# Optimization experiments

Hardware: AMD Instinct MI355X
Metric: run time of the kernel (lower is better)

Reference implementation:

```python
import jax, jax.numpy as jnp
import numpy as np

B, L, D, H, NL = 4, 2048, 128, 4, 2
DH = D // H
FF = 2 * D
EPS_LN = 1e-5


def _p(key, shape, scale=0.05):
    return (jax.random.normal(key, shape, dtype=jnp.float32) * scale)


def setup_inputs() -> dict:
    key = jax.random.key(0)
    ks = jax.random.split(key, 40)
    inp = {
        "local_global": jax.random.normal(ks[0], (B, D), dtype=jnp.float32),
        "task_features": jax.random.normal(ks[1], (B, L, 15), dtype=jnp.float32),
        "privacy_features": jax.random.normal(ks[2], (B, L, 6), dtype=jnp.float32),
        "dag_features": jax.random.normal(ks[3], (B, L, 4), dtype=jnp.float32),
        # float mask in [0,1); values > 0.5 are MASKED (set to -inf) per torch code
        "attn_mask": jax.random.uniform(ks[4], (B, L, L), dtype=jnp.float32),
        # input projections (stored [in, out]; torch Linear does x @ W.T + b)
        "task_W": _p(ks[5], (15, D)), "task_b": jnp.zeros((D,), jnp.float32),
        "priv_W": _p(ks[6], (6, D)), "priv_b": jnp.zeros((D,), jnp.float32),
        "dag_W": _p(ks[7], (4, D)), "dag_b": jnp.zeros((D,), jnp.float32),
        "pre_g": jnp.ones((D,), jnp.float32), "pre_b": jnp.zeros((D,), jnp.float32),
        "post_g": jnp.ones((D,), jnp.float32), "post_b": jnp.zeros((D,), jnp.float32),
        "out_W": _p(ks[8], (D, D)), "out_b": jnp.zeros((D,), jnp.float32),
        # per-layer params stacked on leading NL axis
        "qW": _p(ks[9], (NL, D, D)), "qb": jnp.zeros((NL, D), jnp.float32),
        "kW": _p(ks[10], (NL, D, D)), "kb": jnp.zeros((NL, D), jnp.float32),
        "vW": _p(ks[11], (NL, D, D)), "vb": jnp.zeros((NL, D), jnp.float32),
        "oW": _p(ks[12], (NL, D, D)), "ob": jnp.zeros((NL, D), jnp.float32),
        "n1g": jnp.ones((NL, D), jnp.float32), "n1b": jnp.zeros((NL, D), jnp.float32),
        "n2g": jnp.ones((NL, D), jnp.float32), "n2b": jnp.zeros((NL, D), jnp.float32),
        "f1W": _p(ks[13], (NL, D, FF)), "f1b": jnp.zeros((NL, FF), jnp.float32),
        "f2W": _p(ks[14], (NL, FF, D)), "f2b": jnp.zeros((NL, D), jnp.float32),
    }
    return inp


def _layernorm(x, g, b):
    mu = x.mean(-1, keepdims=True)
    var = ((x - mu) ** 2).mean(-1, keepdims=True)
    return (x - mu) * jax.lax.rsqrt(var + EPS_LN) * g + b


def _attention(x, add_mask, Wq, bq, Wk, bk, Wv, bv, Wo, bo):
    # x: [B,L,D]; add_mask: [B,L,L] additive (0 or -inf)
    def heads(y):
        return y.reshape(B, L, H, DH).transpose(0, 2, 1, 3)  # [B,H,L,DH]
    q = heads(x @ Wq + bq)
    k = heads(x @ Wk + bk)
    v = heads(x @ Wv + bv)
    scale = 1.0 / np.sqrt(DH).astype(np.float32)
    scores = jnp.einsum('bhqd,bhkd->bhqk', q, k) * scale + add_mask[:, None]
    # fully-masked-row diagonal fixup (torch: set diag score to 0 where row max is -inf)
    row_max = scores.max(-1)                       # [B,H,L]
    fully_masked = jnp.isinf(row_max) & (row_max < 0)
    eye = jnp.eye(L, dtype=bool)
    scores = jnp.where(fully_masked[..., None] & eye, 0.0, scores)
    w = jax.nn.softmax(scores, axis=-1)
    # NaN fallback: if any NaN, replace with 1/L and renormalize (applied globally, as torch does)
    has_nan = jnp.isnan(w).any()
    fixed = jnp.nan_to_num(w, nan=1.0 / L)
    fixed = fixed / (fixed.sum(-1, keepdims=True) + 1e-8)
    w = jnp.where(has_nan, fixed, w)
    out = jnp.einsum('bhqk,bhkd->bhqd', w, v)      # [B,H,L,DH]
    out = out.transpose(0, 2, 1, 3).reshape(B, L, D)
    return out @ Wo + bo


def reference(local_global, task_features, privacy_features, dag_features, attn_mask,
              task_W, task_b, priv_W, priv_b, dag_W, dag_b,
              pre_g, pre_b, post_g, post_b, out_W, out_b,
              qW, qb, kW, kb, vW, vb, oW, ob,
              n1g, n1b, n2g, n2b, f1W, f1b, f2W, f2b):
    # normalize mask: >0.5 means masked; fix all-False rows by masking their diagonal (torch quirk)
    mb = attn_mask > 0.5                            # [B,L,L] bool, True = mask out
    need_fix = ~mb.any(-1)                          # [B,L]
    eye = jnp.eye(L, dtype=bool)
    mb = mb | (need_fix[..., None] & eye)
    add_mask = jnp.where(mb, -jnp.inf, 0.0).astype(jnp.float32)

    ctx = (task_features @ task_W + task_b) + (privacy_features @ priv_W + priv_b) \
          + (dag_features @ dag_W + dag_b)
    x = _layernorm(ctx, pre_g, pre_b)
    for i in range(NL):  # eval mode: dropout = identity
        sa = _attention(_layernorm(x, n1g[i], n1b[i]), add_mask,
                        qW[i], qb[i], kW[i], kb[i], vW[i], vb[i], oW[i], ob[i])
        x = x + sa
        h = _layernorm(x, n2g[i], n2b[i])
        ff = jax.nn.gelu(h @ f1W[i] + f1b[i], approximate=False) @ f2W[i] + f2b[i]
        x = x + ff
    enc = _layernorm(x, post_g, post_b)
    global_ctx = enc.mean(axis=1)                   # [B,D]
    fused = global_ctx + 0.1 * local_global
    aligned = fused @ out_W + out_b
    return aligned
```

## Files before the change

kernel.cpp:

```cpp
#include <hip/hip_runtime.h>
#include <hip/hip_bf16.h>

#define DEV __device__ __forceinline__

typedef float f32x4 __attribute__((ext_vector_type(4)));
typedef float f32x16 __attribute__((ext_vector_type(16)));
typedef short s16x8 __attribute__((ext_vector_type(8)));
typedef unsigned short u16x4 __attribute__((ext_vector_type(4)));
typedef __bf16 bf16x8 __attribute__((ext_vector_type(8)));

DEV bf16x8 as_bf16(s16x8 v) { return __builtin_bit_cast(bf16x8, v); }

DEV unsigned short f2bf(float f) {
    union { __hip_bfloat16 h; unsigned short u; } c;
    c.h = __float2bfloat16(f);
    return c.u;
}

DEV unsigned f2bf2(float lo, float hi) {
    unsigned ulo = __builtin_bit_cast(unsigned, lo);
    unsigned uhi = __builtin_bit_cast(unsigned, hi);
    ulo = (ulo + 0x7fffu + ((ulo >> 16) & 1u)) >> 16;
    uhi = (uhi + 0x7fffu + ((uhi >> 16) & 1u)) & 0xffff0000u;
    return ulo | uhi;
}

DEV float wave_sum64(float v) {
#pragma unroll
    for (int m = 1; m < 64; m <<= 1) v += __shfl_xor(v, m, 64);
    return v;
}

DEV int rot3(int r) { return ((r << 1) | (r >> 2)) & 7; }

constexpr float QSCL = (float)(1.4426950408889634 / 5.656854249492381);

__global__ __launch_bounds__(256) void gace_setup_k(
    const float* __restrict__ am, unsigned long long* __restrict__ bits,
    const float* __restrict__ task, const float* __restrict__ priv, const float* __restrict__ dag,
    const float* __restrict__ tW, const float* __restrict__ tb,
    const float* __restrict__ pW, const float* __restrict__ pb,
    const float* __restrict__ dW, const float* __restrict__ db,
    const float* __restrict__ pre_g, const float* __restrict__ pre_b,
    float* __restrict__ x,
    const float* __restrict__ qW, const float* __restrict__ kW,
    const float* __restrict__ vW, const float* __restrict__ oW,
    const float* __restrict__ f1W, const float* __restrict__ f2W,
    const float* __restrict__ qb, const float* __restrict__ kb,
    const float* __restrict__ vb,
    unsigned short* __restrict__ wbf, float* __restrict__ bcat)
{
    const int bx = blockIdx.x;
    const int tid = threadIdx.x, wid = tid >> 6, l = tid & 63;
    if (bx < 2048) {
        const int row = bx * 4 + wid;
        const float* mrow = am + (size_t)row * 2048;
        unsigned long long myword = 0, orAll = 0, andAll = ~0ull;
#pragma unroll 4
        for (int w = 0; w < 32; ++w) {
            unsigned long long bal = __ballot(mrow[w * 64 + l] > 0.5f);
            if (w == l) myword = bal;
            orAll |= bal; andAll &= bal;
        }
        const int lrow = row & 2047;
        const int dw = lrow >> 6, dbit = lrow & 63;
        if (l == dw) {
            if (orAll == 0ull) myword |= (1ull << dbit);
            else if (andAll == ~0ull) myword &= ~(1ull << dbit);
        }
        if (l < 32) bits[(size_t)row * 32 + l] = myword;
        return;
    }
    if (bx < 4096) {
        const int row = (bx - 2048) * 4 + wid;
        const int d0 = l, d1 = l + 64;
        float a0 = tb[d0] + pb[d0] + db[d0];
        float a1 = tb[d1] + pb[d1] + db[d1];
        const float* tf = task + (size_t)row * 15;
#pragma unroll
        for (int j = 0; j < 15; ++j) { const float t = tf[j]; a0 += t * tW[j * 128 + d0]; a1 += t * tW[j * 128 + d1]; }
        const float* pf = priv + (size_t)row * 6;
#pragma unroll
        for (int j = 0; j < 6; ++j) { const float t = pf[j]; a0 += t * pW[j * 128 + d0]; a1 += t * pW[j * 128 + d1]; }
        const float* df = dag + (size_t)row * 4;
#pragma unroll
        for (int j = 0; j < 4; ++j) { const float t = df[j]; a0 += t * dW[j * 128 + d0]; a1 += t * dW[j * 128 + d1]; }
        const float s = wave_sum64(a0 + a1);
        const float mean = s * (1.f / 128.f);
        const float e0 = a0 - mean, e1 = a1 - mean;
        const float s2 = wave_sum64(e0 * e0 + e1 * e1);
        const float rs = rsqrtf(s2 * (1.f / 128.f) + 1e-5f);
        x[(size_t)row * 128 + d0] = e0 * rs * pre_g[d0] + pre_b[d0];
        x[(size_t)row * 128 + d1] = e1 * rs * pre_g[d1] + pre_b[d1];
        return;
    }
    const int bx2 = bx - 4096;
    const int y = bx2 >> 8;
    const int idx = (bx2 & 255) * 256 + tid;
    if (y == 6) {
        if (idx < 2 * 384) {
            const int i = idx / 384, j = idx % 384;
            float v;
            if (j < 128)      v = qb[i * 128 + j] * QSCL;
            else if (j < 256) v = kb[i * 128 + j - 128];
            else              v = vb[i * 128 + j - 256];
            bcat[idx] = v;
        }
        return;
    }
    const float* src; int K_, N_, off; float scl = 1.0f;
    switch (y) {
        case 0:  src = qW;  K_ = 128; N_ = 128; off = 0;      scl = QSCL; break;
        case 1:  src = kW;  K_ = 128; N_ = 128; off = 16384;  break;
        case 2:  src = vW;  K_ = 128; N_ = 128; off = 32768;  break;
        case 3:  src = oW;  K_ = 128; N_ = 128; off = 49152;  break;
        case 4:  src = f1W; K_ = 128; N_ = 256; off = 65536;  break;
        default: src = f2W; K_ = 256; N_ = 128; off = 98304;  break;
    }
    const int per = K_ * N_;
    if (idx >= 2 * per) return;
    const int i = idx / per, rem = idx % per;
    const int n = rem / K_, k = rem % K_;
    wbf[(size_t)i * 131072 + off + n * K_ + k] = f2bf(src[(size_t)i * per + k * N_ + n] * scl);
}

__global__ __launch_bounds__(256) void gace_qkv_k(
    const float* __restrict__ xin,
    const float* __restrict__ gam, const float* __restrict__ bet,
    const unsigned short* __restrict__ Wt,
    const float* __restrict__ bias,
    unsigned short* __restrict__ qk, unsigned short* __restrict__ vtbuf)
{
    const int tid = threadIdx.x;
    const int wid = tid >> 6, l = tid & 63;
    const int g = (l >> 4) & 3, c16 = l & 15;
    const int m0 = blockIdx.x * 64 + wid * 16;
    const int n0 = blockIdx.y * 64;
    const int arow = m0 + c16;

    float v[4][8];
#pragma unroll
    for (int kc = 0; kc < 4; ++kc) {
        const f32x4 a0 = *(const f32x4*)&xin[(size_t)arow * 128 + kc * 32 + 8 * g];
        const f32x4 a1 = *(const f32x4*)&xin[(size_t)arow * 128 + kc * 32 + 8 * g + 4];
#pragma unroll
        for (int e = 0; e < 4; ++e) { v[kc][e] = a0[e]; v[kc][4 + e] = a1[e]; }
    }
    float s = 0.f;
#pragma unroll
    for (int kc = 0; kc < 4; ++kc)
#pragma unroll
        for (int e = 0; e < 8; ++e) s += v[kc][e];
    s += __shfl_xor(s, 16, 64); s += __shfl_xor(s, 32, 64);
    const float mean = s * (1.f / 128.f);
    float s2 = 0.f;
#pragma unroll
    for (int kc = 0; kc < 4; ++kc)
#pragma unroll
        for (int e = 0; e < 8; ++e) { const float d = v[kc][e] - mean; s2 += d * d; }
    s2 += __shfl_xor(s2, 16, 64); s2 += __shfl_xor(s2, 32, 64);
    const float rs = rsqrtf(s2 * (1.f / 128.f) + 1e-5f);
    s16x8 af[4];
#pragma unroll
    for (int kc = 0; kc < 4; ++kc) {
        union { s16x8 v8; unsigned d[4]; } pk;
#pragma unroll
        for (int j = 0; j < 4; ++j) {
            const int col = kc * 32 + 8 * g + 2 * j;
            const float x0 = (v[kc][2 * j] - mean) * rs * gam[col] + bet[col];
            const float x1 = (v[kc][2 * j + 1] - mean) * rs * gam[col + 1] + bet[col + 1];
            pk.d[j] = f2bf2(x0, x1);
        }
        af[kc] = pk.v8;
    }

    f32x4 acc[4];
#pragma unroll
    for (int i = 0; i < 4; ++i) acc[i] = f32x4{0.f, 0.f, 0.f, 0.f};
#pragma unroll
    for (int ns = 0; ns < 4; ++ns) {
        const unsigned short* wrow = Wt + (size_t)(n0 + 16 * ns + c16) * 128;
#pragma unroll
        for (int kc = 0; kc < 4; ++kc) {
            const s16x8 bfv = *(const s16x8*)&wrow[kc * 32 + 8 * g];
            acc[ns] = __builtin_amdgcn_mfma_f32_16x16x32_bf16(
                as_bf16(af[kc]), as_bf16(bfv), acc[ns], 0, 0, 0);
        }
    }
    if (n0 >= 256) {
        const int row0 = m0 + 4 * g;
#pragma unroll
        for (int ns = 0; ns < 4; ++ns) {
            const int n = n0 + ns * 16 + c16;
            const float bv = bias[n];
            u16x4 pk;
#pragma unroll
            for (int r = 0; r < 4; ++r) pk[r] = f2bf(acc[ns][r] + bv);
            *(u16x4*)&vtbuf[(size_t)(n - 256) * 8192 + row0] = pk;
        }
        return;
    }
#pragma unroll
    for (int ns = 0; ns < 4; ++ns) {
        const int n = n0 + ns * 16 + c16;
        const float bv = bias[n];
#pragma unroll
        for (int r = 0; r < 4; ++r)
            qk[(size_t)(m0 + 4 * g + r) * 256 + n] = f2bf(acc[ns][r] + bv);
    }
}

__global__ __launch_bounds__(512) void gace_flash7_k(
    const unsigned short* __restrict__ QK,
    const unsigned short* __restrict__ Vt,
    const unsigned long long* __restrict__ bits,
    float* __restrict__ Op, float* __restrict__ ml)
{
    __shared__ __align__(16) unsigned short Ks[2 * 2 * 2560];
    __shared__ __align__(16) char VtB[2 * 2 * 4096];

    const int tid = threadIdx.x;
    const int wid = tid >> 6, l = tid & 63;
    const int c32 = l & 31, hi = l >> 5;
    const int bid = (blockIdx.x & 7) * 64 + (blockIdx.x >> 3);
    const int split = bid & 3, qc = (bid >> 2) & 7, h = (bid >> 5) & 3, b = bid >> 7;
    const size_t base = (size_t)b * 2048;
    const int qb0 = qc * 256 + wid * 32;
    const int q = qb0 + c32;

    const unsigned short* qrow = &QK[(base + q) * 256 + h * 32];
    const s16x8 qf0 = *(const s16x8*)&qrow[8 * hi];
    const s16x8 qf1 = *(const s16x8*)&qrow[16 + 8 * hi];
    const int rot3c = rot3(c32 & 7);

    f32x16 oacc;
#pragma unroll
    for (int i = 0; i < 16; ++i) oacc[i] = 0.f;
    float l_ = 0.f;

    const int st = tid & 255;
    const int sr = st >> 2;
    const int se = (tid & 3) << 3;
    const int lowr = sr & 31, t12 = lowr & 12;
    const int prow = (sr & 32) | (((t12 == 4) | (t12 == 8)) ? (lowr ^ 12) : lowr);
    const int rv = st >> 3;
    const int sv = tid & 7;
    const int vds = rv * 128 + 16 * (sv ^ rot3(rv & 7));

    const int kv0 = split * 512;
    const unsigned long long* bq = &bits[(base + q) * 32 + split * 8];
    const unsigned short* kgb = &QK[base * 256 + 128 + h * 32 + se];
    const unsigned short* vgb = &Vt[(size_t)(h * 32 + rv) * 8192 + base + kv0 + sv * 8];

    s16x8 kregA, kregB, vregA, vregB;
    auto LOAD = [&](int it2) {
        if (tid < 256) {
            const int kv = kv0 + it2 * 128;
            kregA = *(const s16x8*)&kgb[(size_t)(kv + sr) * 256];
            kregB = *(const s16x8*)&kgb[(size_t)(kv + 64 + sr) * 256];
        } else {
            vregA = *(const s16x8*)&vgb[it2 * 128];
            vregB = *(const s16x8*)&vgb[it2 * 128 + 64];
        }
    };
    auto STAGE = [&](int pb) {
        if (tid < 256) {
            *(s16x8*)&Ks[(pb * 2 + 0) * 2560 + prow * 40 + se] = kregA;
            *(s16x8*)&Ks[(pb * 2 + 1) * 2560 + prow * 40 + se] = kregB;
        } else {
            *(s16x8*)&VtB[(pb * 2 + 0) * 4096 + vds] = vregA;
            *(s16x8*)&VtB[(pb * 2 + 1) * 4096 + vds] = vregB;
        }
    };
    auto COMPUTE = [&](int pb, int sub, unsigned long long wb) {
        const unsigned short* KsS = &Ks[(pb * 2 + sub) * 2560];
        const char* VtS = &VtB[(pb * 2 + sub) * 4096];
        const unsigned long long wbs = wb >> (8 * hi);
        const unsigned wlo = (unsigned)wbs, whiw = (unsigned)(wbs >> 32);
        __builtin_amdgcn_s_setprio(1);
#pragma unroll
        for (int H = 0; H < 2; ++H) {
            const unsigned short* kr = &KsS[(32 * H + c32) * 40 + 8 * hi];
            f32x16 zv;
#pragma unroll
            for (int i = 0; i < 16; ++i) zv[i] = 0.f;
            f32x16 sac = __builtin_amdgcn_mfma_f32_32x32x16_bf16(
                as_bf16(*(const s16x8*)&kr[0]), as_bf16(qf0), zv, 0, 0, 0);
            sac = __builtin_amdgcn_mfma_f32_32x32x16_bf16(
                as_bf16(*(const s16x8*)&kr[16]), as_bf16(qf1), sac, 0, 0, 0);
            const unsigned word = (H == 0) ? wlo : whiw;
#pragma unroll
            for (int ch = 0; ch < 2; ++ch) {
                const int c = 2 * H + ch;
                const int bb = ch * 16;
                float p[8];
#pragma unroll
                for (int e = 0; e < 8; ++e) {
                    const float pe = exp2f(sac[ch * 8 + e]);
                    p[e] = ((word >> (bb + e)) & 1u) ? 0.f : pe;
                }
                l_ += ((p[0] + p[1]) + (p[2] + p[3])) + ((p[4] + p[5]) + (p[6] + p[7]));
                union { s16x8 v; unsigned d[4]; } pa;
#pragma unroll
                for (int j = 0; j < 4; ++j)
                    asm("v_cvt_pk_bf16_f32 %0, %1, %2"
                        : "=v"(pa.d[j]) : "v"(p[2 * j]), "v"(p[2 * j + 1]));
                const s16x8 vf = *(const s16x8*)&VtS[c32 * 128 + 16 * ((2 * c + hi) ^ rot3c)];
                oacc = __builtin_amdgcn_mfma_f32_32x32x16_bf16(
                    as_bf16(pa.v), as_bf16(vf), oacc, 0, 0, 0);
            }
        }
        __builtin_amdgcn_s_setprio(0);
    };

    unsigned long long wbv[8];
#pragma unroll
    for (int w = 0; w < 8; ++w) wbv[w] = bq[w];
    LOAD(0);
    STAGE(0);
    LOAD(1);
    __syncthreads();

#pragma unroll
    for (int it = 0; it < 4; ++it) {
        const int p = it & 1;
        COMPUTE(p, 0, wbv[2 * it]);
        if (it < 3) {
            STAGE(p ^ 1);
            if (it < 2) LOAD(it + 2);
        }
        COMPUTE(p, 1, wbv[2 * it + 1]);
        if (it < 3) __syncthreads();
    }

    l_ += __shfl_xor(l_, 32, 64);
    float* orow = &Op[((size_t)split * 8192 + base + qb0) * 128 + h * 32 + c32];
#pragma unroll
    for (int r = 0; r < 16; ++r) {
        const int qoff = (r & 3) + 8 * (r >> 2) + 4 * hi;
        orow[(size_t)qoff * 128] = oacc[r];
    }
    if (l < 32) ml[((size_t)split * 8192 + base + q) * 4 + h] = l_;
}

template<int QKV, int LAST>
__global__ __launch_bounds__(256) void gace_post2_k(
    const float* __restrict__ Op, const float* __restrict__ ml,
    const unsigned short* __restrict__ oWt, const float* __restrict__ obv,
    float* __restrict__ x,
    const float* __restrict__ n2g, const float* __restrict__ n2b,
    const unsigned short* __restrict__ f1Wt, const float* __restrict__ f1b,
    const unsigned short* __restrict__ f2Wt, const float* __restrict__ f2b,
    const float* __restrict__ n1g2, const float* __restrict__ n1b2,
    const unsigned short* __restrict__ w2, const float* __restrict__ bcat2,
    unsigned short* __restrict__ qk, unsigned short* __restrict__ vtbuf,
    const float* __restrict__ post_g, const float* __restrict__ post_b,
    float* __restrict__ partial)
{
    __shared__ __align__(16) float xbuf[16][132];
    __shared__ __align__(16) unsigned short g1buf[16][264];
    __shared__ float stats[16][2];
    const int tid = threadIdx.x, wid = tid >> 6, l = tid & 63;
    const int g = (l >> 4) & 3, c16 = l & 15;
    const int m0 = blockIdx.x * 16;
    const int arow = m0 + c16;

    s16x8 af[4];
#pragma unroll
    for (int kc = 0; kc < 4; ++kc) {
        float o[8];
#pragma unroll
        for (int e = 0; e < 8; ++e) o[e] = 0.f;
        float Ls = 0.f;
#pragma unroll
        for (int sp = 0; sp < 4; ++sp) {
            const size_t ro = (size_t)sp * 8192 + arow;
            const f32x4 a0 = *(const f32x4*)&Op[ro * 128 + kc * 32 + 8 * g];
            const f32x4 a1 = *(const f32x4*)&Op[ro * 128 + kc * 32 + 8 * g + 4];
#pragma unroll
            for (int e = 0; e < 4; ++e) { o[e] += a0[e]; o[4 + e] += a1[e]; }
            Ls += ml[ro * 4 + kc];
        }
        const float inv = 1.f / Ls;
        union { s16x8 v8; unsigned d[4]; } pk;
#pragma unroll
        for (int j = 0; j < 4; ++j) pk.d[j] = f2bf2(o[2 * j] * inv, o[2 * j + 1] * inv);
        af[kc] = pk.v8;
    }
    {
        f32x4 acc2[2];
#pragma unroll
        for (int z = 0; z < 2; ++z) acc2[z] = f32x4{0.f, 0.f, 0.f, 0.f};
#pragma unroll
        for (int nsl = 0; nsl < 2; ++nsl) {
            const int ns = wid * 2 + nsl;
            const unsigned short* wrow = oWt + (size_t)(16 * ns + c16) * 128;
#pragma unroll
            for (int kc = 0; kc < 4; ++kc)
                acc2[nsl] = __builtin_amdgcn_mfma_f32_16x16x32_bf16(
                    as_bf16(af[kc]), as_bf16(*(const s16x8*)&wrow[kc * 32 + 8 * g]),
                    acc2[nsl], 0, 0, 0);
        }
#pragma unroll
        for (int nsl = 0; nsl < 2; ++nsl) {
            const int n = 16 * (wid * 2 + nsl) + c16;
            const float bv = obv[n];
#pragma unroll
            for (int r = 0; r < 4; ++r) {
                const int lr = 4 * g + r;
                xbuf[lr][n] = acc2[nsl][r] + bv + x[(size_t)(m0 + lr) * 128 + n];
            }
        }
    }
    __syncthreads();
    s16x8 af1[4];
    {
        float v2[4][8];
#pragma unroll
        for (int kc = 0; kc < 4; ++kc) {
            const f32x4 a0 = *(const f32x4*)&xbuf[c16][kc * 32 + 8 * g];
            const f32x4 a1 = *(const f32x4*)&xbuf[c16][kc * 32 + 8 * g + 4];
#pragma unroll
            for (int e = 0; e < 4; ++e) { v2[kc][e] = a0[e]; v2[kc][4 + e] = a1[e]; }
        }
        float s = 0.f;
#pragma unroll
        for (int kc = 0; kc < 4; ++kc)
#pragma unroll
            for (int e = 0; e < 8; ++e) s += v2[kc][e];
        s += __shfl_xor(s, 16, 64); s += __shfl_xor(s, 32, 64);
        const float mean = s * (1.f / 128.f);
        float s2 = 0.f;
#pragma unroll
        for (int kc = 0; kc < 4; ++kc)
#pragma unroll
            for (int e = 0; e < 8; ++e) { const float d = v2[kc][e] - mean; s2 += d * d; }
        s2 += __shfl_xor(s2, 16, 64); s2 += __shfl_xor(s2, 32, 64);
        const float rs = rsqrtf(s2 * (1.f / 128.f) + 1e-5f);
#pragma unroll
        for (int kc = 0; kc < 4; ++kc) {
            union { s16x8 v8; unsigned d[4]; } pk;
#pragma unroll
            for (int j = 0; j < 4; ++j) {
                const int col = kc * 32 + 8 * g + 2 * j;
                const float x0 = (v2[kc][2 * j] - mean) * rs * n2g[col] + n2b[col];
                const float x1 = (v2[kc][2 * j + 1] - mean) * rs * n2g[col + 1] + n2b[col + 1];
                pk.d[j] = f2bf2(x0, x1);
            }
            af1[kc] = pk.v8;
        }
    }
    {
        f32x4 accf[4];
#pragma unroll
        for (int z = 0; z < 4; ++z) accf[z] = f32x4{0.f, 0.f, 0.f, 0.f};
#pragma unroll
        for (int nsl = 0; nsl < 4; ++nsl) {
            const int ns = wid * 4 + nsl;
            const unsigned short* wrow = f1Wt + (size_t)(16 * ns + c16) * 128;
#pragma unroll
            for (int kc = 0; kc < 4; ++kc)
                accf[nsl] = __builtin_amdgcn_mfma_f32_16x16x32_bf16(
                    as_bf16(af1[kc]), as_bf16(*(const s16x8*)&wrow[kc * 32 + 8 * g]),
                    accf[nsl], 0, 0, 0);
        }
#pragma unroll
        for (int nsl = 0; nsl < 4; ++nsl) {
            const int n = 16 * (wid * 4 + nsl) + c16;
            const float bv = f1b[n];
#pragma unroll
            for (int r = 0; r < 4; ++r) {
                float vv = accf[nsl][r] + bv;
                vv = vv * 0.5f * (1.0f + erff(vv * 0.70710678118654752f));
                g1buf[4 * g + r][n] = f2bf(vv);
            }
        }
    }
    __syncthreads();
    float fx[2][4];
    {
        s16x8 af2[8];
#pragma unroll
        for (int kc = 0; kc < 8; ++kc)
            af2[kc] = *(const s16x8*)&g1buf[c16][kc * 32 + 8 * g];
        f32x4 acc2[2];
#pragma unroll
        for (int z = 0; z < 2; ++z) acc2[z] = f32x4{0.f, 0.f, 0.f, 0.f};
#pragma unroll
        for (int nsl = 0; nsl < 2; ++nsl) {
            const int ns = wid * 2 + nsl;
            const unsigned short* wrow = f2Wt + (size_t)(16 * ns + c16) * 256;
#pragma unroll
            for (int kc = 0; kc < 8; ++kc)
                acc2[nsl] = __builtin_amdgcn_mfma_f32_16x16x32_bf16(
                    as_bf16(af2[kc]), as_bf16(*(const s16x8*)&wrow[kc * 32 + 8 * g]),
                    acc2[nsl], 0, 0, 0);
        }
#pragma unroll
        for (int nsl = 0; nsl < 2; ++nsl) {
            const int n = 16 * (wid * 2 + nsl) + c16;
            const float bv = f2b[n];
#pragma unroll
            for (int r = 0; r < 4; ++r)
                fx[nsl][r] = acc2[nsl][r] + bv + xbuf[4 * g + r][n];
        }
    }
    if (!QKV && !LAST) {
#pragma unroll
        for (int nsl = 0; nsl < 2; ++nsl) {
            const int n = 16 * (wid * 2 + nsl) + c16;
#pragma unroll
            for (int r = 0; r < 4; ++r)
                x[(size_t)(m0 + 4 * g + r) * 128 + n] = fx[nsl][r];
        }
        return;
    }
#pragma unroll
    for (int nsl = 0; nsl < 2; ++nsl) {
        const int n = 16 * (wid * 2 + nsl) + c16;
#pragma unroll
        for (int r = 0; r < 4; ++r) {
            const int lr = 4 * g + r;
            if (QKV) x[(size_t)(m0 + lr) * 128 + n] = fx[nsl][r];
            xbuf[lr][n] = fx[nsl][r];
        }
    }
    __syncthreads();
    if (QKV) {
        s16x8 afq[4];
        {
            float v1[4][8];
#pragma unroll
            for (int kc = 0; kc < 4; ++kc) {
                const f32x4 a0 = *(const f32x4*)&xbuf[c16][kc * 32 + 8 * g];
                const f32x4 a1 = *(const f32x4*)&xbuf[c16][kc * 32 + 8 * g + 4];
#pragma unroll
                for (int e = 0; e < 4; ++e) { v1[kc][e] = a0[e]; v1[kc][4 + e] = a1[e]; }
            }
            float s1 = 0.f;
#pragma unroll
            for (int kc = 0; kc < 4; ++kc)
#pragma unroll
                for (int e = 0; e < 8; ++e) s1 += v1[kc][e];
            s1 += __shfl_xor(s1, 16, 64); s1 += __shfl_xor(s1, 32, 64);
            const float mean1 = s1 * (1.f / 128.f);
            float sq1 = 0.f;
#pragma unroll
            for (int kc = 0; kc < 4; ++kc)
#pragma unroll
                for (int e = 0; e < 8; ++e) { const float d = v1[kc][e] - mean1; sq1 += d * d; }
            sq1 += __shfl_xor(sq1, 16, 64); sq1 += __shfl_xor(sq1, 32, 64);
            const float rs1 = rsqrtf(sq1 * (1.f / 128.f) + 1e-5f);
#pragma unroll
            for (int kc = 0; kc < 4; ++kc) {
                union { s16x8 v8; unsigned d[4]; } pk;
#pragma unroll
                for (int j = 0; j < 4; ++j) {
                    const int col = kc * 32 + 8 * g + 2 * j;
                    const float x0 = (v1[kc][2 * j] - mean1) * rs1 * n1g2[col] + n1b2[col];
                    const float x1 = (v1[kc][2 * j + 1] - mean1) * rs1 * n1g2[col + 1] + n1b2[col + 1];
                    pk.d[j] = f2bf2(x0, x1);
                }
                afq[kc] = pk.v8;
            }
        }
#pragma unroll
        for (int j = 0; j < 6; ++j) {
            const int ns = wid * 6 + j;
            const unsigned short* wrow = w2 + (size_t)(ns * 16 + c16) * 128;
            f32x4 acc = f32x4{0.f, 0.f, 0.f, 0.f};
#pragma unroll
            for (int kc = 0; kc < 4; ++kc)
                acc = __builtin_amdgcn_mfma_f32_16x16x32_bf16(
                    as_bf16(afq[kc]), as_bf16(*(const s16x8*)&wrow[kc * 32 + 8 * g]),
                    acc, 0, 0, 0);
            const int n = ns * 16 + c16;
            const float bv = bcat2[n];
            if (ns >= 16) {
                const int row0 = m0 + 4 * g;
                u16x4 pk;
#pragma unroll
                for (int r = 0; r < 4; ++r) pk[r] = f2bf(acc[r] + bv);
                *(u16x4*)&vtbuf[(size_t)(n - 256) * 8192 + row0] = pk;
            } else {
#pragma unroll
                for (int r = 0; r < 4; ++r)
                    qk[(size_t)(m0 + 4 * g + r) * 256 + n] = f2bf(acc[r] + bv);
            }
        }
        return;
    }
    {
#pragma unroll
        for (int rr = 0; rr < 4; ++rr) {
            const int row = wid * 4 + rr;
            const float v0 = xbuf[row][l], v1 = xbuf[row][l + 64];
            const float s = wave_sum64(v0 + v1);
            const float mean = s * (1.f / 128.f);
            const float d0 = v0 - mean, d1 = v1 - mean;
            const float s2 = wave_sum64(d0 * d0 + d1 * d1);
            const float rstd = rsqrtf(s2 * (1.f / 128.f) + 1e-5f);
            if (l == 0) { stats[row][0] = mean; stats[row][1] = rstd; }
        }
        __syncthreads();
#pragma unroll
        for (int nsl = 0; nsl < 2; ++nsl) {
            const int ns = wid * 2 + nsl;
            const int n = 16 * ns + c16;
            const float pg = post_g[n], pb_ = post_b[n];
            float cs = 0.f;
#pragma unroll
            for (int r = 0; r < 4; ++r) {
                const int row = 4 * g + r;
                cs += (xbuf[row][n] - stats[row][0]) * stats[row][1] * pg + pb_;
            }
            cs += __shfl_xor(cs, 16, 64);
            cs += __shfl_xor(cs, 32, 64);
            if (l < 16) partial[(size_t)blockIdx.x * 128 + n] = cs;
        }
    }
}

__global__ __launch_bounds__(128) void gace_tailB_k(
    const float* __restrict__ partial, const float* __restrict__ lg,
    const float* __restrict__ oW, const float* __restrict__ obv,
    float* __restrict__ out)
{
    const int tid = threadIdx.x, b2 = blockIdx.x;
    __shared__ float fused[128];
    float s = 0.f;
#pragma unroll 8
    for (int c = 0; c < 128; ++c) s += partial[(size_t)(b2 * 128 + c) * 128 + tid];
    fused[tid] = s * (1.f / 2048.f) + 0.1f * lg[b2 * 128 + tid];
    __syncthreads();
    float r = obv[tid];
#pragma unroll 8
    for (int d2 = 0; d2 < 128; ++d2) r += fused[d2] * oW[d2 * 128 + tid];
    out[b2 * 128 + tid] = r;
}

extern "C" void kernel_launch(void* const* d_in, const int* in_sizes, int n_in,
                              void* d_out, int out_size, void* d_ws, size_t ws_size,
                              hipStream_t stream)
{
    (void)in_sizes; (void)n_in; (void)out_size; (void)ws_size;
    const float* local_global = (const float*)d_in[0];
    const float* task   = (const float*)d_in[1];
    const float* priv   = (const float*)d_in[2];
    const float* dag    = (const float*)d_in[3];
    const float* amask  = (const float*)d_in[4];
    const float* task_W = (const float*)d_in[5];
    const float* task_b = (const float*)d_in[6];
    const float* priv_W = (const float*)d_in[7];
    const float* priv_b = (const float*)d_in[8];
    const float* dag_W  = (const float*)d_in[9];
    const float* dag_b  = (const float*)d_in[10];
    const float* pre_g  = (const float*)d_in[11];
    const float* pre_b  = (const float*)d_in[12];
    const float* post_g = (const float*)d_in[13];
    const float* post_b = (const float*)d_in[14];
    const float* out_W  = (const float*)d_in[15];
    const float* out_b  = (const float*)d_in[16];
    const float* qW = (const float*)d_in[17];
    const float* qb = (const float*)d_in[18];
    const float* kW = (const float*)d_in[19];
    const float* kb = (const float*)d_in[20];
    const float* vW = (const float*)d_in[21];
    const float* vb = (const float*)d_in[22];
    const float* oW = (const float*)d_in[23];
    const float* ob = (const float*)d_in[24];
    const float* n1g = (const float*)d_in[25];
    const float* n1b = (const float*)d_in[26];
    const float* n2g = (const float*)d_in[27];
    const float* n2b = (const float*)d_in[28];
    const float* f1W = (const float*)d_in[29];
    const float* f1b = (const float*)d_in[30];
    const float* f2W = (const float*)d_in[31];
    const float* f2b = (const float*)d_in[32];

    char* ws = (char*)d_ws;
    size_t off = 0;
    auto carve = [&](size_t sz) {
        void* p = ws + off;
        off += (sz + 255) & ~(size_t)255;
        return p;
    };
    unsigned long long* bits = (unsigned long long*)carve(8192ull * 32 * 8);
    float*          x    = (float*)carve(8192ull * 128 * 4);
    unsigned short* qk   = (unsigned short*)carve(8192ull * 256 * 2);
    unsigned short* vt   = (unsigned short*)carve(128ull * 8192 * 2);
    float*          part = (float*)carve(512ull * 128 * 4);
    float*          Op   = (float*)carve(4ull * 8192 * 128 * 4);
    float*          mlb  = (float*)carve(4ull * 8192 * 4 * 4);
    unsigned short* wbf  = (unsigned short*)carve(2ull * 131072 * 2);
    float*          bcat = (float*)carve(2ull * 384 * 4);

    gace_setup_k<<<5888, 256, 0, stream>>>(
        amask, bits,
        task, priv, dag, task_W, task_b, priv_W, priv_b, dag_W, dag_b,
        pre_g, pre_b, x,
        qW, kW, vW, oW, f1W, f2W, qb, kb, vb, wbf, bcat);
    gace_qkv_k<<<dim3(128, 6), 256, 0, stream>>>(
        x, n1g, n1b, wbf, bcat, qk, vt);
    gace_flash7_k<<<512, 512, 0, stream>>>(qk, vt, bits, Op, mlb);
    gace_post2_k<1, 0><<<512, 256, 0, stream>>>(
        Op, mlb, wbf + 49152, ob, x, n2g, n2b,
        wbf + 65536, f1b, wbf + 98304, f2b,
        n1g + 128, n1b + 128, wbf + 131072, bcat + 384, qk, vt,
        nullptr, nullptr, nullptr);
    gace_flash7_k<<<512, 512, 0, stream>>>(qk, vt, bits, Op, mlb);
    gace_post2_k<0, 1><<<512, 256, 0, stream>>>(
        Op, mlb, wbf + 131072 + 49152, ob + 128, x, n2g + 128, n2b + 128,
        wbf + 131072 + 65536, f1b + 256, wbf + 131072 + 98304, f2b + 128,
        nullptr, nullptr, nullptr, nullptr, nullptr, nullptr,
        post_g, post_b, part);
    gace_tailB_k<<<4, 128, 0, stream>>>(part, local_global, out_W, out_b, (float*)d_out);
}
```

Measured before the change: 160.7 us.

## Split flash attention KV into 8 chunks and store partial outputs in bf16

The attention kernel now splits each query block's key range into 8 chunks of 256 instead of 4 chunks of 512, doubling the grid to 1024 blocks for more parallelism and shorter per-block pipelines. To keep the partial-output traffic in check, the unnormalized partial outputs are written as bf16 rather than fp32, and the post kernel sums 8 bf16 partials per element. This trades extra reduction reads and reduced precision in the partials for better GPU occupancy and a shorter per-block KV loop.

After: 157.8 us. Within noise of the previous version (-1.8%).

```diff
diff --git a/kernel.cpp b/kernel.cpp
--- a/kernel.cpp
+++ b/kernel.cpp
@@ -15,6 +15,10 @@
     union { __hip_bfloat16 h; unsigned short u; } c;
     c.h = __float2bfloat16(f);
     return c.u;
+}
+
+DEV float bf2f(unsigned short u) {
+    return __builtin_bit_cast(float, (unsigned)u << 16);
 }
 
 DEV unsigned f2bf2(float lo, float hi) {
@@ -210,11 +214,11 @@
     }
 }
 
-__global__ __launch_bounds__(512) void gace_flash7_k(
+__global__ __launch_bounds__(512) void gace_flash8_k(
     const unsigned short* __restrict__ QK,
     const unsigned short* __restrict__ Vt,
     const unsigned long long* __restrict__ bits,
-    float* __restrict__ Op, float* __restrict__ ml)
+    unsigned short* __restrict__ Opb, float* __restrict__ ml)
 {
     __shared__ __align__(16) unsigned short Ks[2 * 2 * 2560];
     __shared__ __align__(16) char VtB[2 * 2 * 4096];
@@ -222,8 +226,8 @@
     const int tid = threadIdx.x;
     const int wid = tid >> 6, l = tid & 63;
     const int c32 = l & 31, hi = l >> 5;
-    const int bid = (blockIdx.x & 7) * 64 + (blockIdx.x >> 3);
-    const int split = bid & 3, qc = (bid >> 2) & 7, h = (bid >> 5) & 3, b = bid >> 7;
+    const int bid = (blockIdx.x & 7) * 128 + (blockIdx.x >> 3);
+    const int split = bid & 7, qc = (bid >> 3) & 7, h = (bid >> 6) & 3, b = bid >> 8;
     const size_t base = (size_t)b * 2048;
     const int qb0 = qc * 256 + wid * 32;
     const int q = qb0 + c32;
@@ -247,8 +251,8 @@
     const int sv = tid & 7;
     const int vds = rv * 128 + 16 * (sv ^ rot3(rv & 7));
 
-    const int kv0 = split * 512;
-    const unsigned long long* bq = &bits[(base + q) * 32 + split * 8];
+    const int kv0 = split * 256;
+    const unsigned long long* bq = &bits[(base + q) * 32 + split * 4];
     const unsigned short* kgb = &QK[base * 256 + 128 + h * 32 + se];
     const unsigned short* vgb = &Vt[(size_t)(h * 32 + rv) * 8192 + base + kv0 + sv * 8];
 
@@ -313,39 +317,36 @@
         __builtin_amdgcn_s_setprio(0);
     };
 
-    unsigned long long wbv[8];
-#pragma unroll
-    for (int w = 0; w < 8; ++w) wbv[w] = bq[w];
+    unsigned long long wbv[4];
+#pragma unroll
+    for (int w = 0; w < 4; ++w) wbv[w] = bq[w];
     LOAD(0);
     STAGE(0);
     LOAD(1);
     __syncthreads();
 
 #pragma unroll
-    for (int it = 0; it < 4; ++it) {
+    for (int it = 0; it < 2; ++it) {
         const int p = it & 1;
         COMPUTE(p, 0, wbv[2 * it]);
-        if (it < 3) {
-            STAGE(p ^ 1);
-            if (it < 2) LOAD(it + 2);
-        }
+        if (it < 1) STAGE(p ^ 1);
         COMPUTE(p, 1, wbv[2 * it + 1]);
-        if (it < 3) __syncthreads();
+        if (it < 1) __syncthreads();
     }
 
     l_ += __shfl_xor(l_, 32, 64);
-    float* orow = &Op[((size_t)split * 8192 + base + qb0) * 128 + h * 32 + c32];
+    unsigned short* orow = &Opb[((size_t)split * 8192 + base + qb0) * 128 + h * 32 + c32];
 #pragma unroll
     for (int r = 0; r < 16; ++r) {
         const int qoff = (r & 3) + 8 * (r >> 2) + 4 * hi;
-        orow[(size_t)qoff * 128] = oacc[r];
+        orow[(size_t)qoff * 128] = f2bf(oacc[r]);
     }
     if (l < 32) ml[((size_t)split * 8192 + base + q) * 4 + h] = l_;
 }
 
 template<int QKV, int LAST>
 __global__ __launch_bounds__(256) void gace_post2_k(
-    const float* __restrict__ Op, const float* __restrict__ ml,
+    const unsigned short* __restrict__ Opb, const float* __restrict__ ml,
     const unsigned short* __restrict__ oWt, const float* __restrict__ obv,
     float* __restrict__ x,
     const float* __restrict__ n2g, const float* __restrict__ n2b,
@@ -373,12 +374,12 @@
         for (int e = 0; e < 8; ++e) o[e] = 0.f;
         float Ls = 0.f;
 #pragma unroll
-        for (int sp = 0; sp < 4; ++sp) {
+        for (int sp = 0; sp < 8; ++sp) {
             const size_t ro = (size_t)sp * 8192 + arow;
-            const f32x4 a0 = *(const f32x4*)&Op[ro * 128 + kc * 32 + 8 * g];
-            const f32x4 a1 = *(const f32x4*)&Op[ro * 128 + kc * 32 + 8 * g + 4];
-#pragma unroll
-            for (int e = 0; e < 4; ++e) { o[e] += a0[e]; o[4 + e] += a1[e]; }
+            union { s16x8 v; unsigned short u[8]; } ov;
+            ov.v = *(const s16x8*)&Opb[ro * 128 + kc * 32 + 8 * g];
+#pragma unroll
+            for (int e = 0; e < 8; ++e) o[e] += bf2f(ov.u[e]);
             Ls += ml[ro * 4 + kc];
         }
         const float inv = 1.f / Ls;
@@ -690,8 +691,8 @@
     unsigned short* qk   = (unsigned short*)carve(8192ull * 256 * 2);
     unsigned short* vt   = (unsigned short*)carve(128ull * 8192 * 2);
     float*          part = (float*)carve(512ull * 128 * 4);
-    float*          Op   = (float*)carve(4ull * 8192 * 128 * 4);
-    float*          mlb  = (float*)carve(4ull * 8192 * 4 * 4);
+    unsigned short* Opb  = (unsigned short*)carve(8ull * 8192 * 128 * 2);
+    float*          mlb  = (float*)carve(8ull * 8192 * 4 * 4);
     unsigned short* wbf  = (unsigned short*)carve(2ull * 131072 * 2);
     float*          bcat = (float*)carve(2ull * 384 * 4);
 
@@ -702,15 +703,15 @@
         qW, kW, vW, oW, f1W, f2W, qb, kb, vb, wbf, bcat);
     gace_qkv_k<<<dim3(128, 6), 256, 0, stream>>>(
         x, n1g, n1b, wbf, bcat, qk, vt);
-    gace_flash7_k<<<512, 512, 0, stream>>>(qk, vt, bits, Op, mlb);
+    gace_flash8_k<<<1024, 512, 0, stream>>>(qk, vt, bits, Opb, mlb);
     gace_post2_k<1, 0><<<512, 256, 0, stream>>>(
-        Op, mlb, wbf + 49152, ob, x, n2g, n2b,
+        Opb, mlb, wbf + 49152, ob, x, n2g, n2b,
         wbf + 65536, f1b, wbf + 98304, f2b,
         n1g + 128, n1b + 128, wbf + 131072, bcat + 384, qk, vt,
         nullptr, nullptr, nullptr);
-    gace_flash7_k<<<512, 512, 0, stream>>>(qk, vt, bits, Op, mlb);
+    gace_flash8_k<<<1024, 512, 0, stream>>>(qk, vt, bits, Opb, mlb);
     gace_post2_k<0, 1><<<512, 256, 0, stream>>>(
-        Op, mlb, wbf + 131072 + 49152, ob + 128, x, n2g + 128, n2b + 128,
+        Opb, mlb, wbf + 131072 + 49152, ob + 128, x, n2g + 128, n2b + 128,
         wbf + 131072 + 65536, f1b + 256, wbf + 131072 + 98304, f2b + 128,
         nullptr, nullptr, nullptr, nullptr, nullptr, nullptr,
         post_g, post_b, part);
```
